# Performance work log

Hardware: AMD Instinct MI355X
Metric: run time of the kernel (lower is better)

Reference implementation:

```python
import jax, jax.numpy as jnp
import numpy as np

N = 4096      # sequence length (tokens)
D = 256       # model_dim
H = 4         # num_heads
DH = D // H   # dim_per_head = 64
TOPK = 30     # dot_attention default
SCALE = float((DH // H) ** -0.5)  # torch: (key.size(-1)//num_heads)**-0.5 = 16**-0.5 = 0.25
LN_EPS = 1e-5


def setup_inputs() -> dict:
    key = jax.random.key(0)
    ks = jax.random.split(key, 11)
    s = 0.02
    return {
        "key_in":   jax.random.normal(ks[0], (N, D), jnp.float32),
        "value_in": jax.random.normal(ks[1], (N, D), jnp.float32),
        "query_in": jax.random.normal(ks[2], (N, D), jnp.float32),
        "Wq": jax.random.normal(ks[3], (D, D), jnp.float32) * s,
        "bq": jax.random.normal(ks[4], (D,), jnp.float32) * s,
        "Wk": jax.random.normal(ks[5], (D, D), jnp.float32) * s,
        "bk": jax.random.normal(ks[6], (D,), jnp.float32) * s,
        "Wv": jax.random.normal(ks[7], (D, D), jnp.float32) * s,
        "bv": jax.random.normal(ks[8], (D,), jnp.float32) * s,
        "Wo": jax.random.normal(ks[9], (D, D), jnp.float32) * s,
        "bo": jax.random.normal(ks[10], (D,), jnp.float32) * s,
        "ln_g": jnp.ones((D,), jnp.float32),
        "ln_b": jnp.zeros((D,), jnp.float32),
    }


def reference(key_in, value_in, query_in, Wq, bq, Wk, bk, Wv, bv, Wo, bo, ln_g, ln_b):
    # Projections (nn.Linear: x @ W.T + b)
    q = query_in @ Wq.T + bq            # (N, D)
    k = key_in @ Wk.T + bk
    v = value_in @ Wv.T + bv
    # view(N, H, DH).transpose(0,1) -> (H, N, DH)
    qh = q.reshape(N, H, DH).transpose(1, 0, 2)
    kh = k.reshape(N, H, DH).transpose(1, 0, 2)
    vh = v.reshape(N, H, DH).transpose(1, 0, 2)

    scores = jnp.einsum('hnd,hmd->hnm', qh, kh) * SCALE   # (H, N, N)

    # top-k mask via scatter (faithful to torch.topk + scatter_)
    idx = jax.lax.top_k(scores, TOPK)[1]                  # (H, N, TOPK)
    mask = jnp.zeros_like(scores).at[
        jnp.arange(H)[:, None, None],
        jnp.arange(N)[None, :, None],
        idx].set(1.0)
    masked = jnp.where(mask > 0, scores, -jnp.inf)
    attn = jax.nn.softmax(masked, axis=-1)                # (H, N, N); dropout p=0 -> identity

    ctx = jnp.einsum('hnm,hmd->hnd', attn, vh)            # (H, N, DH)
    ctx = ctx.transpose(1, 0, 2).reshape(N, D)

    out = ctx @ Wo.T + bo
    resid = query_in + out                                # residual is pre-projection query
    mu = resid.mean(axis=-1, keepdims=True)
    var = resid.var(axis=-1, keepdims=True)               # biased var, like torch LayerNorm
    out = (resid - mu) / jnp.sqrt(var + LN_EPS) * ln_g + ln_b
    return out, attn
```

## Files before the change

kernel.cpp:

```cpp
#include <hip/hip_runtime.h>
#include <stdint.h>

#define N_TOK 4096
#define DIM   256
#define NH    4
#define DH    64
#define TOPK  30
#define CANDN 40
#define ATT_SCALE 0.25f
#define LN_EPS 1e-5f

typedef __attribute__((ext_vector_type(8))) short bf16x8;
typedef __attribute__((ext_vector_type(4))) float f32x4;

static __device__ __forceinline__ ushort f2bf(float f) {
    uint x = __float_as_uint(f);
    return (ushort)((x + 0x7FFFu + ((x >> 16) & 1u)) >> 16);
}
static __device__ __forceinline__ bf16x8 load_frag(const ushort* p) {
    union { int4 i; bf16x8 f; } u;
    u.i = *reinterpret_cast<const int4*>(p);
    return u.f;
}
static __device__ __forceinline__ uint s16key(uint u) {
    return (u & 0x8000u) ? (u ^ 0xFFFFu) : (u | 0x8000u);
}

#define BK 32
__global__ __launch_bounds__(256) void qk_gemm_f32(
    const float* __restrict__ query_in, const float* __restrict__ key_in,
    const float* __restrict__ Wq, const float* __restrict__ bq,
    const float* __restrict__ Wk, const float* __restrict__ bk,
    float* __restrict__ qf, float* __restrict__ kf,
    ushort* __restrict__ qb, ushort* __restrict__ kb)
{
    const int j0g = blockIdx.x * 64;
    const int sel = j0g >> 8;
    const int j0  = j0g & 255;
    const float* A    = sel ? key_in : query_in;
    const float* W    = sel ? Wk : Wq;
    const float* bias = sel ? bk : bq;
    float*  outF = sel ? kf : qf;
    ushort* outB = sel ? kb : qb;

    __shared__ float As[BK][64 + 4];
    __shared__ float Ws[BK][64 + 4];
    const int tid = threadIdx.x;
    const int tx = tid & 15;
    const int ty = tid >> 4;
    const int i0 = blockIdx.y * 64;

    float acc[4][4];
#pragma unroll
    for (int r = 0; r < 4; r++)
#pragma unroll
        for (int c = 0; c < 4; c++) acc[r][c] = 0.f;

    for (int k0 = 0; k0 < DIM; k0 += BK) {
#pragma unroll
        for (int u = 0; u < 2; u++) {
            const int f = u * 256 + tid;
            const int r = f >> 3;
            const int c = (f & 7) * 4;
            float4 va = *reinterpret_cast<const float4*>(A + (size_t)(i0 + r) * DIM + k0 + c);
            As[c + 0][r] = va.x; As[c + 1][r] = va.y;
            As[c + 2][r] = va.z; As[c + 3][r] = va.w;
            float4 vw = *reinterpret_cast<const float4*>(W + (size_t)(j0 + r) * DIM + k0 + c);
            Ws[c + 0][r] = vw.x; Ws[c + 1][r] = vw.y;
            Ws[c + 2][r] = vw.z; Ws[c + 3][r] = vw.w;
        }
        __syncthreads();
#pragma unroll
        for (int kk = 0; kk < BK; kk++) {
            const float4 a4 = *reinterpret_cast<const float4*>(&As[kk][ty * 4]);
            const float4 b4 = *reinterpret_cast<const float4*>(&Ws[kk][tx * 4]);
            const float ar[4] = {a4.x, a4.y, a4.z, a4.w};
            const float br[4] = {b4.x, b4.y, b4.z, b4.w};
#pragma unroll
            for (int r = 0; r < 4; r++)
#pragma unroll
                for (int c = 0; c < 4; c++) acc[r][c] += ar[r] * br[c];
        }
        __syncthreads();
    }

#pragma unroll
    for (int r = 0; r < 4; r++) {
        const int gi = i0 + ty * 4 + r;
#pragma unroll
        for (int c = 0; c < 4; c++) {
            const int gj = j0 + tx * 4 + c;
            float v = acc[r][c] + bias[gj];
            outF[(size_t)gi * DIM + gj] = v;
            outB[(size_t)gi * DIM + gj] = f2bf(v);
        }
    }
}

__global__ __launch_bounds__(256) void cast_kernel(
    const float* __restrict__ value_in, const float* __restrict__ Wv,
    const float* __restrict__ Wo, ushort* __restrict__ value_b,
    ushort* __restrict__ Wv_b, ushort* __restrict__ Wo_b)
{
    const int id4 = blockIdx.x * 256 + threadIdx.x;
    const int NV = 1048576 / 4, NW = 65536 / 4;
    const float* src; ushort* dst; int off;
    if (id4 < NV)            { src = value_in; dst = value_b; off = id4; }
    else if (id4 < NV + NW)  { src = Wv; dst = Wv_b; off = id4 - NV; }
    else                     { src = Wo; dst = Wo_b; off = id4 - NV - NW; }
    float4 v = reinterpret_cast<const float4*>(src)[off];
    ushort4 o = {f2bf(v.x), f2bf(v.y), f2bf(v.z), f2bf(v.w)};
    reinterpret_cast<ushort4*>(dst)[off] = o;
}

__global__ __launch_bounds__(256) void mfma_gemm(
    const ushort* __restrict__ A, const ushort* __restrict__ B,
    const float* __restrict__ bias, const float* __restrict__ addX,
    float* __restrict__ outF)
{
    const int lane = threadIdx.x & 63;
    const int wv   = threadIdx.x >> 6;
    const int i0   = blockIdx.y * 64 + wv * 16;
    const int j0   = blockIdx.x * 64;
    const int r = lane & 15, q = lane >> 4;

    f32x4 acc[4];
#pragma unroll
    for (int b = 0; b < 4; b++) acc[b] = (f32x4){0.f, 0.f, 0.f, 0.f};

#pragma unroll
    for (int ks = 0; ks < 8; ks++) {
        const int kk = ks * 32 + q * 8;
        bf16x8 af = load_frag(A + (size_t)(i0 + r) * DIM + kk);
        bf16x8 bfr[4];
#pragma unroll
        for (int jt = 0; jt < 4; jt++)
            bfr[jt] = load_frag(B + (size_t)(j0 + jt * 16 + r) * DIM + kk);
#pragma unroll
        for (int jt = 0; jt < 4; jt++)
            acc[jt] = __builtin_amdgcn_mfma_f32_16x16x32_bf16(af, bfr[jt], acc[jt], 0, 0, 0);
    }

#pragma unroll
    for (int jt = 0; jt < 4; jt++) {
        const int gj = j0 + jt * 16 + r;
        const float bv = bias[gj];
#pragma unroll
        for (int rg = 0; rg < 4; rg++) {
            const int gi = i0 + q * 4 + rg;
            float v = acc[jt][rg] + bv;
            if (addX) v += addX[(size_t)gi * DIM + gj];
            outF[(size_t)gi * DIM + gj] = v;
        }
    }
}

__global__ __launch_bounds__(256) void scores_kernel(
    const ushort* __restrict__ qb, const ushort* __restrict__ kb,
    ushort* __restrict__ sb)
{
    const int lane = threadIdx.x & 63;
    const int wv   = threadIdx.x >> 6;
    const int h    = blockIdx.z;
    const int i0   = blockIdx.y * 128 + wv * 32;
    const int j0   = blockIdx.x * 128;
    const int r = lane & 15, q = lane >> 4;
    const int koff = h * DH;

    f32x4 acc[2][8];
#pragma unroll
    for (int a = 0; a < 2; a++)
#pragma unroll
        for (int b = 0; b < 8; b++) acc[a][b] = (f32x4){0.f, 0.f, 0.f, 0.f};

#pragma unroll
    for (int ks = 0; ks < 2; ks++) {
        const int kk = koff + ks * 32 + q * 8;
        bf16x8 af[2], bfr[8];
#pragma unroll
        for (int mt = 0; mt < 2; mt++)
            af[mt] = load_frag(qb + (size_t)(i0 + mt * 16 + r) * DIM + kk);
#pragma unroll
        for (int jt = 0; jt < 8; jt++)
            bfr[jt] = load_frag(kb + (size_t)(j0 + jt * 16 + r) * DIM + kk);
#pragma unroll
        for (int mt = 0; mt < 2; mt++)
#pragma unroll
            for (int jt = 0; jt < 8; jt++)
                acc[mt][jt] = __builtin_amdgcn_mfma_f32_16x16x32_bf16(
                    af[mt], bfr[jt], acc[mt][jt], 0, 0, 0);
    }

#pragma unroll
    for (int mt = 0; mt < 2; mt++)
#pragma unroll
        for (int rg = 0; rg < 4; rg++) {
            const int gi = i0 + mt * 16 + q * 4 + rg;
            ushort* row = sb + ((size_t)(h * N_TOK + gi)) * N_TOK;
#pragma unroll
            for (int jt = 0; jt < 8; jt++)
                row[j0 + jt * 16 + r] = (ushort)s16key(f2bf(acc[mt][jt][rg]));
        }
}

__global__ __launch_bounds__(256) void select_kernel(
    const ushort* __restrict__ sb, const float* __restrict__ qf,
    const float* __restrict__ kf, const float* __restrict__ vf,
    float* __restrict__ pval, int* __restrict__ pidx,
    ushort* __restrict__ ctxb)
{
    const int lane = threadIdx.x & 63;
    const int wv   = threadIdx.x >> 6;
    const int row  = blockIdx.x * 4 + wv;
    const int h    = row >> 12;
    const int i    = row & (N_TOK - 1);
    const ushort* srow = sb + (size_t)row * N_TOK;

    __shared__ uint  hist[4][256];
    __shared__ uint  cand[4][64];
    __shared__ uint  ccnt[4];
    __shared__ float pw[4][TOPK];
    __shared__ int   jw[4][TOPK];
    __shared__ __align__(16) float qsh[4][DH];

    qsh[wv][lane] = qf[(size_t)i * DIM + h * DH + lane];
    if (lane == 0) ccnt[wv] = 0;
#pragma unroll
    for (int b = 0; b < 4; b++) hist[wv][b * 64 + lane] = 0u;

    uint kw[32];
    const int4* srow4 = reinterpret_cast<const int4*>(srow);
#pragma unroll
    for (int t = 0; t < 8; t++) {
        int4 c = srow4[t * 64 + lane];
        kw[t * 4 + 0] = (uint)c.x; kw[t * 4 + 1] = (uint)c.y;
        kw[t * 4 + 2] = (uint)c.z; kw[t * 4 + 3] = (uint)c.w;
    }

    uint mx = 0;
#pragma unroll
    for (int w = 0; w < 32; w++) {
        uint lo16 = kw[w] & 0xFFFFu, hi16 = kw[w] >> 16;
        mx = max(mx, max(lo16, hi16));
    }
#pragma unroll
    for (int off = 32; off; off >>= 1)
        mx = max(mx, (uint)__shfl_xor((int)mx, off));

    __syncthreads();

#pragma unroll
    for (int w = 0; w < 32; w++) {
        uint d0 = mx - (kw[w] & 0xFFFFu);
        uint d1 = mx - (kw[w] >> 16);
        if (d0 < 255u) atomicAdd(&hist[wv][d0], 1u);
        if (d1 < 255u) atomicAdd(&hist[wv][d1], 1u);
    }
    __syncthreads();

    const uint c0 = hist[wv][lane * 4 + 0];
    const uint c1 = hist[wv][lane * 4 + 1];
    const uint c2 = hist[wv][lane * 4 + 2];
    const uint c3 = hist[wv][lane * 4 + 3];
    const uint seg = c0 + c1 + c2 + c3;
    uint scan = seg;
#pragma unroll
    for (int d = 1; d < 64; d <<= 1) {
        uint y = (uint)__shfl_up((int)scan, d);
        if (lane >= d) scan += y;
    }
    const uint excl = scan - seg;
    const bool crossing = (excl < CANDN) && (scan >= CANDN);
    unsigned long long bal = __ballot(crossing);

    int t = 256;
    if (bal != 0ull) {
        const int srcLane = __ffsll(bal) - 1;
        int tloc = lane * 4;
        if (crossing) {
            uint cum = excl + c0;
            if (cum < CANDN) { tloc++; cum += c1;
                if (cum < CANDN) { tloc++; cum += c2;
                    if (cum < CANDN) { tloc++; } } }
        }
        t = __shfl(tloc, srcLane);
    }

    uint T;
    if (t <= 254) {
        T = mx - (uint)t;
    } else {
        uint lo = 0;
#pragma unroll
        for (int b = 15; b >= 0; b--) {
            uint trial = lo | (1u << b);
            int c = 0;
#pragma unroll
            for (int w = 0; w < 32; w++) {
                c += ((kw[w] & 0xFFFFu) >= trial) ? 1 : 0;
                c += ((kw[w] >> 16)     >= trial) ? 1 : 0;
            }
#pragma unroll
            for (int off = 32; off; off >>= 1) c += __shfl_xor(c, off);
            if (c >= CANDN) lo = trial;
        }
        T = lo;
    }

#pragma unroll
    for (int w = 0; w < 32; w++) {
        const uint lo16 = kw[w] & 0xFFFFu, hi16 = kw[w] >> 16;
        const int jbase = (w >> 2) * 512 + lane * 8 + (w & 3) * 2;
        if (lo16 >= T) {
            uint pos = atomicAdd(&ccnt[wv], 1u);
            if (pos < 64u) cand[wv][pos] = (uint)jbase;
        }
        if (hi16 >= T) {
            uint pos = atomicAdd(&ccnt[wv], 1u);
            if (pos < 64u) cand[wv][pos] = (uint)(jbase + 1);
        }
    }
    __syncthreads();
    const int m = (int)min(ccnt[wv], 64u);

    unsigned long long ukey = 0ull;
    if (lane < m) {
        const int j = (int)cand[wv][lane];
        const float4* kr = reinterpret_cast<const float4*>(kf + (size_t)j * DIM + h * DH);
        const float4* qr = reinterpret_cast<const float4*>(qsh[wv]);
        float s = 0.f;
#pragma unroll
        for (int d = 0; d < 16; d++) {
            float4 a = qr[d], bb = kr[d];
            s += a.x * bb.x; s += a.y * bb.y; s += a.z * bb.z; s += a.w * bb.w;
        }
        uint bits = __float_as_uint(s);
        uint s32 = (bits & 0x80000000u) ? ~bits : (bits | 0x80000000u);
        ukey = ((unsigned long long)s32 << 12) | (unsigned long long)(4095 - j);
    }

#pragma unroll
    for (int k = 2; k <= 64; k <<= 1) {
#pragma unroll
        for (int jj = k >> 1; jj > 0; jj >>= 1) {
            unsigned long long o = __shfl_xor(ukey, jj);
            bool keepMax = ((lane & jj) != 0) ^ ((lane & k) != 0);
            ukey = keepMax ? (ukey > o ? ukey : o) : (ukey < o ? ukey : o);
        }
    }

    const int rank = 63 - lane;
    const int jsel = 4095 - (int)(ukey & 0xFFFull);
    uint s32b = (uint)(ukey >> 12);
    uint fb = (s32b & 0x80000000u) ? (s32b ^ 0x80000000u) : ~s32b;
    const float sc = __uint_as_float(fb);
    const float stop = __shfl(sc, 63);

    float e = (rank < TOPK) ? __expf((sc - stop) * ATT_SCALE) : 0.f;
    float esum = e;
#pragma unroll
    for (int off = 32; off; off >>= 1) esum += __shfl_xor(esum, off);
    const float p = e / esum;

    if (rank < TOPK) {
        pw[wv][rank] = p; jw[wv][rank] = jsel;
        pval[(size_t)row * 32 + rank] = p;
        pidx[(size_t)row * 32 + rank] = jsel;
    }
    __syncthreads();

    float a = 0.f;
#pragma unroll
    for (int c = 0; c < TOPK; c++)
        a += pw[wv][c] * vf[(size_t)jw[wv][c] * DIM + h * DH + lane];
    ctxb[(size_t)i * DIM + h * DH + lane] = f2bf(a);
}

__global__ __launch_bounds__(256) void attn_write(
    const float* __restrict__ pval, const int* __restrict__ pidx,
    float* __restrict__ attnF)
{
    __shared__ __align__(16) float rb[4][N_TOK];
    const int tid = threadIdx.x;
    const int r0 = blockIdx.x * 4;

    float4* rb4 = reinterpret_cast<float4*>(&rb[0][0]);
    const float4 z = {0.f, 0.f, 0.f, 0.f};
#pragma unroll
    for (int t = 0; t < 16; t++) rb4[t * 256 + tid] = z;
    __syncthreads();
    if (tid < 4 * TOPK) {
        const int w = tid / TOPK, c = tid % TOPK;
        rb[w][pidx[(size_t)(r0 + w) * 32 + c]] = pval[(size_t)(r0 + w) * 32 + c];
    }
    __syncthreads();
#pragma unroll
    for (int w = 0; w < 4; w++) {
        float4* grow = reinterpret_cast<float4*>(attnF + (size_t)(r0 + w) * N_TOK);
#pragma unroll
        for (int t = 0; t < 4; t++)
            grow[t * 256 + tid] = rb4[w * 1024 + t * 256 + tid];
    }
}

__global__ __launch_bounds__(64) void ln_kernel(
    float* __restrict__ resb, const float* __restrict__ g,
    const float* __restrict__ b)
{
    const int i = blockIdx.x, lane = threadIdx.x;
    float4* rowp = reinterpret_cast<float4*>(resb + (size_t)i * DIM);
    float4 x = rowp[lane];
    float s  = x.x + x.y + x.z + x.w;
    float sq = x.x * x.x + x.y * x.y + x.z * x.z + x.w * x.w;
#pragma unroll
    for (int off = 32; off; off >>= 1) {
        s  += __shfl_xor(s, off);
        sq += __shfl_xor(sq, off);
    }
    const float mu  = s * (1.f / DIM);
    const float var = sq * (1.f / DIM) - mu * mu;
    const float rstd = rsqrtf(var + LN_EPS);
    const int col = lane * 4;
    float4 o;
    o.x = (x.x - mu) * rstd * g[col + 0] + b[col + 0];
    o.y = (x.y - mu) * rstd * g[col + 1] + b[col + 1];
    o.z = (x.z - mu) * rstd * g[col + 2] + b[col + 2];
    o.w = (x.w - mu) * rstd * g[col + 3] + b[col + 3];
    rowp[lane] = o;
}

extern "C" void kernel_launch(void* const* d_in, const int* in_sizes, int n_in,
                              void* d_out, int out_size, void* d_ws, size_t ws_size,
                              hipStream_t stream)
{
    const float* key_in   = (const float*)d_in[0];
    const float* value_in = (const float*)d_in[1];
    const float* query_in = (const float*)d_in[2];
    const float* Wq = (const float*)d_in[3];
    const float* bq = (const float*)d_in[4];
    const float* Wk = (const float*)d_in[5];
    const float* bk = (const float*)d_in[6];
    const float* Wv = (const float*)d_in[7];
    const float* bv = (const float*)d_in[8];
    const float* Wo = (const float*)d_in[9];
    const float* bo = (const float*)d_in[10];
    const float* ln_g = (const float*)d_in[11];
    const float* ln_b = (const float*)d_in[12];

    float* outF  = (float*)d_out;
    float* attnF = outF + (size_t)N_TOK * DIM;

    const size_t SC = 33554432;
    ushort* sb   = (ushort*)attnF;
    float*  qf   = attnF + SC;
    float*  kf   = attnF + SC + 1048576;
    float*  vf   = attnF + SC + 2097152;
    ushort* qb   = (ushort*)(attnF + SC + 3145728);
    ushort* kb   = (ushort*)(attnF + SC + 3670016);
    ushort* ctxb = (ushort*)(attnF + SC + 4194304);

    float*  pval    = (float*)d_ws;
    int*    pidx    = (int*)d_ws + 524288;
    ushort* value_b = (ushort*)((char*)d_ws + (4u << 20));
    ushort* Wv_b    = (ushort*)((char*)d_ws + (6u << 20));
    ushort* Wo_b    = (ushort*)((char*)d_ws + (6u << 20) + 131072);

    cast_kernel<<<dim3((1048576 + 65536 + 65536) / 4 / 256), 256, 0, stream>>>(
        value_in, Wv, Wo, value_b, Wv_b, Wo_b);
    qk_gemm_f32<<<dim3(8, 64), 256, 0, stream>>>(
        query_in, key_in, Wq, bq, Wk, bk, qf, kf, qb, kb);
    mfma_gemm<<<dim3(4, 64), 256, 0, stream>>>(value_b, Wv_b, bv, nullptr, vf);

    scores_kernel<<<dim3(32, 32, NH), 256, 0, stream>>>(qb, kb, sb);
    select_kernel<<<dim3(N_TOK * NH / 4), 256, 0, stream>>>(
        sb, qf, kf, vf, pval, pidx, ctxb);

    mfma_gemm<<<dim3(4, 64), 256, 0, stream>>>(ctxb, Wo_b, bo, query_in, outF);
    ln_kernel<<<N_TOK, 64, 0, stream>>>(outF, ln_g, ln_b);

    attn_write<<<N_TOK * NH / 4, 256, 0, stream>>>(pval, pidx, attnF);
}
```

Before: 440.0 us.

## Fuse score GEMM and top-k selection into one kernel with LDS-resident rows

Merges the bf16 score GEMM and the per-row top-k select into a single 1024-thread kernel. Each block computes a 16x4096 score tile per head directly into swizzled shared memory, and each wave then selects from its own row. This removes the write and read of the 128 MB bf16 score matrix in global memory. The histogram window shrinks to 128 bins, and block barriers become wave barriers. The cost is 128 KB of LDS per block, which gives low occupancy, plus more fallbacks to the binary-search path when the threshold falls outside the smaller window.

```diff
diff --git a/kernel.cpp b/kernel.cpp
--- a/kernel.cpp
+++ b/kernel.cpp
@@ -7,6 +7,7 @@
 #define DH    64
 #define TOPK  30
 #define CANDN 40
+#define HWIN  128u
 #define ATT_SCALE 0.25f
 #define LN_EPS 1e-5f
 
@@ -155,84 +156,64 @@
     }
 }
 
-__global__ __launch_bounds__(256) void scores_kernel(
+__global__ __launch_bounds__(1024) void fused_scores_select(
     const ushort* __restrict__ qb, const ushort* __restrict__ kb,
-    ushort* __restrict__ sb)
+    const float* __restrict__ qf, const float* __restrict__ kf,
+    const float* __restrict__ vf,
+    float* __restrict__ pval, int* __restrict__ pidx,
+    ushort* __restrict__ ctxb)
 {
     const int lane = threadIdx.x & 63;
     const int wv   = threadIdx.x >> 6;
-    const int h    = blockIdx.z;
-    const int i0   = blockIdx.y * 128 + wv * 32;
-    const int j0   = blockIdx.x * 128;
+    const int h    = blockIdx.y;
+    const int i0   = blockIdx.x * 16;
     const int r = lane & 15, q = lane >> 4;
     const int koff = h * DH;
 
-    f32x4 acc[2][8];
-#pragma unroll
-    for (int a = 0; a < 2; a++)
-#pragma unroll
-        for (int b = 0; b < 8; b++) acc[a][b] = (f32x4){0.f, 0.f, 0.f, 0.f};
-
-#pragma unroll
-    for (int ks = 0; ks < 2; ks++) {
-        const int kk = koff + ks * 32 + q * 8;
-        bf16x8 af[2], bfr[8];
-#pragma unroll
-        for (int mt = 0; mt < 2; mt++)
-            af[mt] = load_frag(qb + (size_t)(i0 + mt * 16 + r) * DIM + kk);
-#pragma unroll
-        for (int jt = 0; jt < 8; jt++)
-            bfr[jt] = load_frag(kb + (size_t)(j0 + jt * 16 + r) * DIM + kk);
-#pragma unroll
-        for (int mt = 0; mt < 2; mt++)
-#pragma unroll
-            for (int jt = 0; jt < 8; jt++)
-                acc[mt][jt] = __builtin_amdgcn_mfma_f32_16x16x32_bf16(
-                    af[mt], bfr[jt], acc[mt][jt], 0, 0, 0);
-    }
-
-#pragma unroll
-    for (int mt = 0; mt < 2; mt++)
-#pragma unroll
-        for (int rg = 0; rg < 4; rg++) {
-            const int gi = i0 + mt * 16 + q * 4 + rg;
-            ushort* row = sb + ((size_t)(h * N_TOK + gi)) * N_TOK;
-#pragma unroll
-            for (int jt = 0; jt < 8; jt++)
-                row[j0 + jt * 16 + r] = (ushort)s16key(f2bf(acc[mt][jt][rg]));
-        }
-}
-
-__global__ __launch_bounds__(256) void select_kernel(
-    const ushort* __restrict__ sb, const float* __restrict__ qf,
-    const float* __restrict__ kf, const float* __restrict__ vf,
-    float* __restrict__ pval, int* __restrict__ pidx,
-    ushort* __restrict__ ctxb)
-{
-    const int lane = threadIdx.x & 63;
-    const int wv   = threadIdx.x >> 6;
-    const int row  = blockIdx.x * 4 + wv;
-    const int h    = row >> 12;
-    const int i    = row & (N_TOK - 1);
-    const ushort* srow = sb + (size_t)row * N_TOK;
-
-    __shared__ uint  hist[4][256];
-    __shared__ uint  cand[4][64];
-    __shared__ uint  ccnt[4];
-    __shared__ float pw[4][TOPK];
-    __shared__ int   jw[4][TOPK];
-    __shared__ __align__(16) float qsh[4][DH];
-
-    qsh[wv][lane] = qf[(size_t)i * DIM + h * DH + lane];
-    if (lane == 0) ccnt[wv] = 0;
-#pragma unroll
-    for (int b = 0; b < 4; b++) hist[wv][b * 64 + lane] = 0u;
+    __shared__ __align__(16) ushort sc[16][4096];
+    __shared__ uint  hist[16][HWIN];
+    __shared__ uint  cand[16][64];
+    __shared__ uint  ccnt[16];
+    __shared__ float pw[16][TOPK];
+    __shared__ int   jw[16][TOPK];
+    __shared__ __align__(16) float qsh[16][DH];
+
+    char* const scb = reinterpret_cast<char*>(&sc[0][0]);
+
+    const bf16x8 bq0 = load_frag(qb + (size_t)(i0 + r) * DIM + koff + q * 8);
+    const bf16x8 bq1 = load_frag(qb + (size_t)(i0 + r) * DIM + koff + 32 + q * 8);
+    const uint wswz  = ((uint)(r & 7)) << 4;
+    const uint wbase = (uint)r * 8192u;
+#pragma unroll
+    for (int jt = 0; jt < 16; jt++) {
+        const int jbase = wv * 256 + jt * 16;
+        bf16x8 ka0 = load_frag(kb + (size_t)(jbase + r) * DIM + koff + q * 8);
+        bf16x8 ka1 = load_frag(kb + (size_t)(jbase + r) * DIM + koff + 32 + q * 8);
+        f32x4 acc = (f32x4){0.f, 0.f, 0.f, 0.f};
+        acc = __builtin_amdgcn_mfma_f32_16x16x32_bf16(ka0, bq0, acc, 0, 0, 0);
+        acc = __builtin_amdgcn_mfma_f32_16x16x32_bf16(ka1, bq1, acc, 0, 0, 0);
+        const uint k0 = s16key(f2bf(acc[0])), k1 = s16key(f2bf(acc[1]));
+        const uint k2 = s16key(f2bf(acc[2])), k3 = s16key(f2bf(acc[3]));
+        uint2 two; two.x = k0 | (k1 << 16); two.y = k2 | (k3 << 16);
+        const uint e2 = (uint)((jbase + q * 4) * 2);
+        *reinterpret_cast<uint2*>(scb + (wbase + (e2 ^ wswz))) = two;
+    }
+
+    qsh[wv][lane] = qf[(size_t)(i0 + wv) * DIM + koff + lane];
+    hist[wv][lane] = 0u; hist[wv][64 + lane] = 0u;
+    if (lane == 0) ccnt[wv] = 0u;
+    __syncthreads();
+
+    const int grow = i0 + wv;
+    const int orow = h * N_TOK + grow;
+    const uint rswz = ((uint)(wv & 7)) << 4;
+    char* const rowb = scb + (size_t)wv * 8192;
 
     uint kw[32];
-    const int4* srow4 = reinterpret_cast<const int4*>(srow);
 #pragma unroll
     for (int t = 0; t < 8; t++) {
-        int4 c = srow4[t * 64 + lane];
+        int4 c = *reinterpret_cast<const int4*>(
+            rowb + (((uint)(t * 1024 + lane * 16)) ^ rswz));
         kw[t * 4 + 0] = (uint)c.x; kw[t * 4 + 1] = (uint)c.y;
         kw[t * 4 + 2] = (uint)c.z; kw[t * 4 + 3] = (uint)c.w;
     }
@@ -247,22 +228,18 @@
     for (int off = 32; off; off >>= 1)
         mx = max(mx, (uint)__shfl_xor((int)mx, off));
 
-    __syncthreads();
-
 #pragma unroll
     for (int w = 0; w < 32; w++) {
         uint d0 = mx - (kw[w] & 0xFFFFu);
         uint d1 = mx - (kw[w] >> 16);
-        if (d0 < 255u) atomicAdd(&hist[wv][d0], 1u);
-        if (d1 < 255u) atomicAdd(&hist[wv][d1], 1u);
-    }
-    __syncthreads();
-
-    const uint c0 = hist[wv][lane * 4 + 0];
-    const uint c1 = hist[wv][lane * 4 + 1];
-    const uint c2 = hist[wv][lane * 4 + 2];
-    const uint c3 = hist[wv][lane * 4 + 3];
-    const uint seg = c0 + c1 + c2 + c3;
+        if (d0 < HWIN) atomicAdd(&hist[wv][d0], 1u);
+        if (d1 < HWIN) atomicAdd(&hist[wv][d1], 1u);
+    }
+    __builtin_amdgcn_wave_barrier();
+
+    const uint c0 = hist[wv][lane * 2 + 0];
+    const uint c1 = hist[wv][lane * 2 + 1];
+    const uint seg = c0 + c1;
     uint scan = seg;
 #pragma unroll
     for (int d = 1; d < 64; d <<= 1) {
@@ -276,12 +253,10 @@
     int t = 256;
     if (bal != 0ull) {
         const int srcLane = __ffsll(bal) - 1;
-        int tloc = lane * 4;
+        int tloc = lane * 2;
         if (crossing) {
             uint cum = excl + c0;
-            if (cum < CANDN) { tloc++; cum += c1;
-                if (cum < CANDN) { tloc++; cum += c2;
-                    if (cum < CANDN) { tloc++; } } }
+            if (cum < CANDN) tloc++;
         }
         t = __shfl(tloc, srcLane);
     }
@@ -310,23 +285,23 @@
 #pragma unroll
     for (int w = 0; w < 32; w++) {
         const uint lo16 = kw[w] & 0xFFFFu, hi16 = kw[w] >> 16;
-        const int jbase = (w >> 2) * 512 + lane * 8 + (w & 3) * 2;
+        const int j0c = (w >> 2) * 512 + lane * 8 + (w & 3) * 2;
         if (lo16 >= T) {
             uint pos = atomicAdd(&ccnt[wv], 1u);
-            if (pos < 64u) cand[wv][pos] = (uint)jbase;
+            if (pos < 64u) cand[wv][pos] = (uint)j0c;
         }
         if (hi16 >= T) {
             uint pos = atomicAdd(&ccnt[wv], 1u);
-            if (pos < 64u) cand[wv][pos] = (uint)(jbase + 1);
-        }
-    }
-    __syncthreads();
+            if (pos < 64u) cand[wv][pos] = (uint)(j0c + 1);
+        }
+    }
+    __builtin_amdgcn_wave_barrier();
     const int m = (int)min(ccnt[wv], 64u);
 
     unsigned long long ukey = 0ull;
     if (lane < m) {
         const int j = (int)cand[wv][lane];
-        const float4* kr = reinterpret_cast<const float4*>(kf + (size_t)j * DIM + h * DH);
+        const float4* kr = reinterpret_cast<const float4*>(kf + (size_t)j * DIM + koff);
         const float4* qr = reinterpret_cast<const float4*>(qsh[wv]);
         float s = 0.f;
 #pragma unroll
@@ -353,10 +328,10 @@
     const int jsel = 4095 - (int)(ukey & 0xFFFull);
     uint s32b = (uint)(ukey >> 12);
     uint fb = (s32b & 0x80000000u) ? (s32b ^ 0x80000000u) : ~s32b;
-    const float sc = __uint_as_float(fb);
-    const float stop = __shfl(sc, 63);
-
-    float e = (rank < TOPK) ? __expf((sc - stop) * ATT_SCALE) : 0.f;
+    const float sc2 = __uint_as_float(fb);
+    const float stop = __shfl(sc2, 63);
+
+    float e = (rank < TOPK) ? __expf((sc2 - stop) * ATT_SCALE) : 0.f;
     float esum = e;
 #pragma unroll
     for (int off = 32; off; off >>= 1) esum += __shfl_xor(esum, off);
@@ -364,16 +339,16 @@
 
     if (rank < TOPK) {
         pw[wv][rank] = p; jw[wv][rank] = jsel;
-        pval[(size_t)row * 32 + rank] = p;
-        pidx[(size_t)row * 32 + rank] = jsel;
-    }
-    __syncthreads();
+        pval[(size_t)orow * 32 + rank] = p;
+        pidx[(size_t)orow * 32 + rank] = jsel;
+    }
+    __builtin_amdgcn_wave_barrier();
 
     float a = 0.f;
 #pragma unroll
     for (int c = 0; c < TOPK; c++)
-        a += pw[wv][c] * vf[(size_t)jw[wv][c] * DIM + h * DH + lane];
-    ctxb[(size_t)i * DIM + h * DH + lane] = f2bf(a);
+        a += pw[wv][c] * vf[(size_t)jw[wv][c] * DIM + koff + lane];
+    ctxb[(size_t)grow * DIM + koff + lane] = f2bf(a);
 }
 
 __global__ __launch_bounds__(256) void attn_write(
@@ -451,7 +426,6 @@
     float* attnF = outF + (size_t)N_TOK * DIM;
 
     const size_t SC = 33554432;
-    ushort* sb   = (ushort*)attnF;
     float*  qf   = attnF + SC;
     float*  kf   = attnF + SC + 1048576;
     float*  vf   = attnF + SC + 2097152;
@@ -471,9 +445,8 @@
         query_in, key_in, Wq, bq, Wk, bk, qf, kf, qb, kb);
     mfma_gemm<<<dim3(4, 64), 256, 0, stream>>>(value_b, Wv_b, bv, nullptr, vf);
 
-    scores_kernel<<<dim3(32, 32, NH), 256, 0, stream>>>(qb, kb, sb);
-    select_kernel<<<dim3(N_TOK * NH / 4), 256, 0, stream>>>(
-        sb, qf, kf, vf, pval, pidx, ctxb);
+    fused_scores_select<<<dim3(N_TOK / 16, NH), 1024, 0, stream>>>(
+        qb, kb, qf, kf, vf, pval, pidx, ctxb);
 
     mfma_gemm<<<dim3(4, 64), 256, 0, stream>>>(ctxb, Wo_b, bo, query_in, outF);
     ln_kernel<<<N_TOK, 64, 0, stream>>>(outF, ln_g, ln_b);
```

New measurement: 469.2 us. 6.6% more time.
